# Kernel tuning notes

Hardware: AMD Instinct MI355X
Metric: run time of the kernel (lower is better)

## Reference

```python
import jax, jax.numpy as jnp
import numpy as np

N, E, B = 20000, 320000, 64
IN_DIM, HID, HEADS, NGF = 128, 64, 4, 9
NEG_SLOPE = 0.2
SET2SET_STEPS = 3


def _gat_conv(x, src, dst, W, a_src, a_dst, b, n):
    # PyG GATConv (eval mode): h = xW split into heads, edge score =
    # LeakyReLU(a_src.h[src] + a_dst.h[dst]), softmax over edges per dst node,
    # weighted scatter-sum of h[src], heads concatenated, + bias.
    H, C = a_src.shape
    h = (x @ W).reshape(n, H, C)                       # [N,H,C]
    s = jnp.sum(h * a_src, axis=-1)                    # [N,H]
    d = jnp.sum(h * a_dst, axis=-1)                    # [N,H]
    e = jax.nn.leaky_relu(s[src] + d[dst], NEG_SLOPE)  # [E,H]
    emax = jax.ops.segment_max(e, dst, num_segments=n)
    ex = jnp.exp(e - emax[dst])
    denom = jax.ops.segment_sum(ex, dst, num_segments=n)
    alpha = ex / (denom[dst] + 1e-16)                  # [E,H]
    out = jax.ops.segment_sum(h[src] * alpha[..., None], dst, num_segments=n)
    return out.reshape(n, H * C) + b


def _set2set(x, batch, Wih, Whh, bih, bhh, n_graphs):
    # Set2Set pooling: LSTM(q_star) -> attention over nodes per graph -> readout.
    d = x.shape[1]
    h = jnp.zeros((n_graphs, d), x.dtype)
    c = jnp.zeros((n_graphs, d), x.dtype)
    q_star = jnp.zeros((n_graphs, 2 * d), x.dtype)
    for _ in range(SET2SET_STEPS):
        gates = q_star @ Wih.T + bih + h @ Whh.T + bhh   # [B,4d], torch gate order i,f,g,o
        i, f, g, o = jnp.split(gates, 4, axis=1)
        c = jax.nn.sigmoid(f) * c + jax.nn.sigmoid(i) * jnp.tanh(g)
        h = jax.nn.sigmoid(o) * jnp.tanh(c)
        q = h                                            # [B,d]
        e = jnp.sum(x * q[batch], axis=-1)               # [N]
        emax = jax.ops.segment_max(e, batch, num_segments=n_graphs)
        a = jnp.exp(e - emax[batch])
        a = a / (jax.ops.segment_sum(a, batch, num_segments=n_graphs)[batch] + 1e-16)
        r = jax.ops.segment_sum(a[:, None] * x, batch, num_segments=n_graphs)  # [B,d]
        q_star = jnp.concatenate([q, r], axis=1)
    return q_star


def setup_inputs() -> dict:
    key = jax.random.key(0)
    ks = jax.random.split(key, 20)
    sc = 0.1
    inp = {
        "x": jax.random.normal(ks[0], (N, IN_DIM), jnp.float32),
        "edge_index": jax.random.randint(ks[1], (2, E), 0, N, dtype=jnp.int32),
        "batch": jnp.sort(jax.random.randint(ks[2], (N,), 0, B, dtype=jnp.int32)),
        "graph_features": jax.random.normal(ks[3], (B, NGF), jnp.float32),
        "W1": sc * jax.random.normal(ks[4], (IN_DIM, HEADS * HID), jnp.float32),
        "a_src1": sc * jax.random.normal(ks[5], (HEADS, HID), jnp.float32),
        "a_dst1": sc * jax.random.normal(ks[6], (HEADS, HID), jnp.float32),
        "b1": jnp.zeros((HEADS * HID,), jnp.float32),
        "W2": sc * jax.random.normal(ks[7], (HEADS * HID, HEADS * HID), jnp.float32),
        "a_src2": sc * jax.random.normal(ks[8], (HEADS, HID), jnp.float32),
        "a_dst2": sc * jax.random.normal(ks[9], (HEADS, HID), jnp.float32),
        "b2": jnp.zeros((HEADS * HID,), jnp.float32),
        "W3": sc * jax.random.normal(ks[10], (HEADS * HID, 2 * HID), jnp.float32),
        "a_src3": sc * jax.random.normal(ks[11], (1, 2 * HID), jnp.float32),
        "a_dst3": sc * jax.random.normal(ks[12], (1, 2 * HID), jnp.float32),
        "b3": jnp.zeros((2 * HID,), jnp.float32),
        "Wih": sc * jax.random.normal(ks[13], (4 * 2 * HID, 4 * HID), jnp.float32),
        "Whh": sc * jax.random.normal(ks[14], (4 * 2 * HID, 2 * HID), jnp.float32),
        "bih": jnp.zeros((4 * 2 * HID,), jnp.float32),
        "bhh": jnp.zeros((4 * 2 * HID,), jnp.float32),
        "gW1": sc * jax.random.normal(ks[15], (NGF, HID), jnp.float32),
        "gb1": jnp.zeros((HID,), jnp.float32),
        "gW2": sc * jax.random.normal(ks[16], (HID, HID // 2), jnp.float32),
        "gb2": jnp.zeros((HID // 2,), jnp.float32),
        "mW1": sc * jax.random.normal(ks[17], (2 * (2 * HID) + HID // 2, 128), jnp.float32),
        "mb1": jnp.zeros((128,), jnp.float32),
        "mW2": sc * jax.random.normal(ks[18], (128, 4), jnp.float32),
        "mb2": jnp.zeros((4,), jnp.float32),
    }
    return inp


def reference(x, edge_index, batch, graph_features,
              W1, a_src1, a_dst1, b1,
              W2, a_src2, a_dst2, b2,
              W3, a_src3, a_dst3, b3,
              Wih, Whh, bih, bhh,
              gW1, gb1, gW2, gb2,
              mW1, mb1, mW2, mb2):
    n = x.shape[0]
    # PyG GATConv default add_self_loops=True
    loops = jnp.arange(n, dtype=edge_index.dtype)
    src = jnp.concatenate([edge_index[0], loops])
    dst = jnp.concatenate([edge_index[1], loops])
    h = jax.nn.elu(_gat_conv(x, src, dst, W1, a_src1, a_dst1, b1, n))
    h = jax.nn.elu(_gat_conv(h, src, dst, W2, a_src2, a_dst2, b2, n))
    h = jax.nn.elu(_gat_conv(h, src, dst, W3, a_src3, a_dst3, b3, n))
    pooled = _set2set(h, batch, Wih, Whh, bih, bhh, B)              # [B, 256]
    gf = jax.nn.relu(graph_features @ gW1 + gb1) @ gW2 + gb2        # [B, 32]
    z = jnp.concatenate([pooled, gf], axis=1)                       # [B, 288]
    scores = jax.nn.relu(z @ mW1 + mb1) @ mW2 + mb2                 # [B, 4]
    return scores
```

## Files before the change

### kernel.cpp

```cpp
#include <hip/hip_runtime.h>
#include <hip/hip_bf16.h>
#include <math.h>

#define NEG_SLOPE 0.2f

typedef __attribute__((ext_vector_type(8))) short bf16x8;
typedef __attribute__((ext_vector_type(4))) float f32x4;

__device__ __forceinline__ float sigmoidf(float x){ return 1.f/(1.f+expf(-x)); }
__device__ __forceinline__ float bf2f(unsigned us){ return __uint_as_float(us << 16); }

__device__ __forceinline__ unsigned pack_split(float v){
  __hip_bfloat16 hi = __float2bfloat16(v);
  float rem = v - __bfloat162float(hi);
  __hip_bfloat16 lo = __float2bfloat16(rem);
  unsigned short uh = __builtin_bit_cast(unsigned short, hi);
  unsigned short ul = __builtin_bit_cast(unsigned short, lo);
  return (unsigned)uh | ((unsigned)ul << 16);
}
__device__ __forceinline__ unsigned short bf16of(float v){
  __hip_bfloat16 h = __float2bfloat16(v);
  return __builtin_bit_cast(unsigned short, h);
}

__global__ void init_kernel(int* counts, int* gstart, int* gend,
                            float* rsum, float* lsum, float* sdbuf,
                            int* pad1, int* pad2, int npadints,
                            const float* __restrict__ W1, unsigned* __restrict__ WT1,
                            const float* __restrict__ W2, unsigned* __restrict__ WT2,
                            const float* __restrict__ W3, unsigned* __restrict__ WT3,
                            int n, int b){
  int i = blockIdx.x*blockDim.x + threadIdx.x;
  if (i < n) counts[i] = 0;
  if (i < b){ gstart[i] = 0; gend[i] = 0; }
  if (i < 3*b*128) rsum[i] = 0.f;
  if (i < 3*b) lsum[i] = 0.f;
  if (i < 18*n) sdbuf[i] = 0.f;
  if (i < npadints){ pad1[i] = 0; pad2[i] = 0; }
  if (i < 128*256){
    int k = i>>8, c = i&255;
    WT1[(size_t)c*128 + k] = pack_split(W1[i]);
  }
  if (i < 256*256){
    int k = i>>8, c = i&255;
    WT2[(size_t)c*256 + k] = pack_split(W2[i]);
  }
  if (i < 256*128){
    int k = i>>7, c = i&127;
    WT3[(size_t)c*256 + k] = pack_split(W3[i]);
  }
}

__global__ void build_kernel(const int* __restrict__ ei, const int* __restrict__ batch,
                             int* counts, int* gstart, int* gend, int E, int n){
  int i = blockIdx.x*blockDim.x + threadIdx.x;
  if (i < E) atomicAdd(&counts[ei[E+i]], 1);
  if (i < n){
    int b = batch[i];
    if (i == 0 || batch[i-1] != b) gstart[b] = i;
    if (i == n-1 || batch[i+1] != b) gend[b] = i+1;
  }
}

__global__ void scan_kernel(const int* __restrict__ counts, int* offs, int* cursor, int n){
  const int T = 1024;
  int tid = threadIdx.x;
  int chunk = (n + T - 1)/T;
  int base = tid*chunk;
  int local = 0;
  for (int i=0;i<chunk;i++){ int idx=base+i; if (idx<n) local += counts[idx]; }
  __shared__ int ss[T];
  ss[tid]=local; __syncthreads();
  for (int off=1; off<T; off<<=1){
    int v = (tid>=off)? ss[tid-off] : 0;
    __syncthreads();
    ss[tid]+=v;
    __syncthreads();
  }
  int run = ss[tid]-local;
  for (int i=0;i<chunk;i++){
    int idx=base+i;
    if (idx<n){ offs[idx]=run; cursor[idx]=run; run += counts[idx]; }
  }
  if (tid==T-1) offs[n]=run;
}

__global__ void fill_kernel(const int* __restrict__ ei, int* cursor, int* csr, int E){
  int i = blockIdx.x*blockDim.x + threadIdx.x;
  if (i<E){
    int dst = ei[E+i];
    int pos = atomicAdd(&cursor[dst],1);
    csr[pos] = ei[i];
  }
}

template<bool AF32, int H>
__global__ __launch_bounds__(256) void gemm_bf16(
    const void* __restrict__ Aptr, const short* __restrict__ BT,
    unsigned short* __restrict__ Cb16,
    const float* __restrict__ asrc, const float* __restrict__ adst,
    float* __restrict__ sv, float* __restrict__ dv,
    int M, int Ktot, int N){
  __shared__ short As[64][72];
  __shared__ short Bs[128][72];
  int tid = threadIdx.x;
  int wave = tid>>6, lane = tid&63;
  int quad = lane>>4, l16 = lane&15;
  int bm = blockIdx.y*64, bn = blockIdx.x*128;
  f32x4 acc[8];
  #pragma unroll
  for (int i=0;i<8;i++) acc[i] = (f32x4){0.f,0.f,0.f,0.f};
  int rr = tid>>3;
  int seg = (tid&7)*8;
  int4 ra[2], rb[4];
  auto loadAB = [&](int k0){
    if (AF32){
      const float* A = (const float*)Aptr;
      int Kf = Ktot>>1;
      int fo = (k0+seg)>>1;
      #pragma unroll
      for (int p=0;p<2;p++){
        int row = bm + p*32 + rr;
        float4 v = make_float4(0.f,0.f,0.f,0.f);
        if (row < M) v = *(const float4*)(A + (size_t)row*Kf + fo);
        ra[p] = make_int4((int)pack_split(v.x),(int)pack_split(v.y),
                          (int)pack_split(v.z),(int)pack_split(v.w));
      }
    } else {
      const short* A = (const short*)Aptr;
      #pragma unroll
      for (int p=0;p<2;p++)
        ra[p] = *(const int4*)(A + (size_t)(bm + p*32 + rr)*Ktot + k0 + seg);
    }
    #pragma unroll
    for (int p=0;p<4;p++)
      rb[p] = *(const int4*)(BT + (size_t)(bn + p*32 + rr)*Ktot + k0 + seg);
  };
  loadAB(0);
  for (int k0=0; k0<Ktot; k0+=64){
    __syncthreads();
    #pragma unroll
    for (int p=0;p<2;p++) *(int4*)&As[p*32+rr][seg] = ra[p];
    #pragma unroll
    for (int p=0;p<4;p++) *(int4*)&Bs[p*32+rr][seg] = rb[p];
    __syncthreads();
    if (k0+64 < Ktot) loadAB(k0+64);
    #pragma unroll
    for (int kk=0;kk<2;kk++){
      bf16x8 af = *(bf16x8*)&As[wave*16 + l16][kk*32 + quad*8];
      #pragma unroll
      for (int nf=0;nf<8;nf++){
        bf16x8 bfv = *(bf16x8*)&Bs[nf*16 + l16][kk*32 + quad*8];
        acc[nf] = __builtin_amdgcn_mfma_f32_16x16x32_bf16(af, bfv, acc[nf], 0,0,0);
      }
    }
  }
  float av[8], bv[8];
  #pragma unroll
  for (int nf=0;nf<8;nf++){
    int c = bn + nf*16 + l16;
    av[nf] = asrc[c];
    bv[nf] = adst[c];
  }
  #pragma unroll
  for (int r=0;r<4;r++){
    int row = bm + wave*16 + quad*4 + r;
    float psA=0.f, pdA=0.f, psB=0.f, pdB=0.f;
    #pragma unroll
    for (int nf=0;nf<4;nf++){ psA += acc[nf][r]*av[nf]; pdA += acc[nf][r]*bv[nf]; }
    #pragma unroll
    for (int nf=4;nf<8;nf++){ psB += acc[nf][r]*av[nf]; pdB += acc[nf][r]*bv[nf]; }
    #pragma unroll
    for (int off=1; off<16; off<<=1){
      psA += __shfl_xor(psA,off); pdA += __shfl_xor(pdA,off);
      psB += __shfl_xor(psB,off); pdB += __shfl_xor(pdB,off);
    }
    if (l16==0 && row < M){
      if (H == 4){
        int h0 = bn>>6;
        atomicAdd(&sv[row*4 + h0],     psA);
        atomicAdd(&dv[row*4 + h0],     pdA);
        atomicAdd(&sv[row*4 + h0 + 1], psB);
        atomicAdd(&dv[row*4 + h0 + 1], pdB);
      } else {
        atomicAdd(&sv[row], psA + psB);
        atomicAdd(&dv[row], pdA + pdB);
      }
    }
  }
  __syncthreads();
  unsigned short* stg = (unsigned short*)(&As[0][0]) + wave*528;
  #pragma unroll
  for (int r=0;r<4;r++){
    #pragma unroll
    for (int nf=0;nf<8;nf++)
      stg[quad*132 + nf*16 + l16] = bf16of(acc[nf][r]);
    #pragma unroll
    for (int p=0;p<4;p++){
      int row = bm + wave*16 + p*4 + r;
      if (row < M){
        unsigned v = (unsigned)stg[p*132 + lane*2] |
                     ((unsigned)stg[p*132 + lane*2 + 1] << 16);
        *(unsigned*)(Cb16 + (size_t)row*N + bn + lane*2) = v;
      }
    }
  }
}

template<int H, int C, bool SPLIT>
__global__ __launch_bounds__(256) void agg_kernel(
    const unsigned short* __restrict__ hb, const float* __restrict__ s,
    const float* __restrict__ d, const int* __restrict__ offs,
    const int* __restrict__ csr, const float* __restrict__ bias,
    float* __restrict__ yf, unsigned* __restrict__ ys, int n_nodes){
  constexpr int HC = H*C;
  constexpr int VEC = HC/64;
  int n = blockIdx.x;
  int tid = threadIdx.x;
  int wave = tid>>6, lane = tid&63;
  __shared__ float sdst[H];
  __shared__ float sl[H];
  __shared__ float sw[64*H];
  __shared__ int ssrc[64];
  __shared__ float facc[4][HC];
  if (tid < H) sdst[tid] = d[n*H+tid];
  int start = offs[n];
  int cnt = offs[n+1]-start;
  int cnt1 = cnt+1;
  __syncthreads();
  float acc[VEC] = {};
  float lp[H];
  #pragma unroll
  for (int h=0;h<H;h++) lp[h]=0.f;
  for (int base=0; base<cnt1; base+=64){
    int nchunk = min(64, cnt1-base);
    if (tid < nchunk){
      int i = base+tid;
      int src = (i==cnt) ? n : csr[start+i];
      ssrc[tid]=src;
      if (H == 4){
        float4 sv = *reinterpret_cast<const float4*>(s + (size_t)src*4);
        float ev[4] = {sv.x, sv.y, sv.z, sv.w};
        #pragma unroll
        for (int h=0;h<4;h++){
          float e = ev[h] + sdst[h];
          e = e>=0.f ? e : NEG_SLOPE*e;
          float w = expf(e);
          sw[tid*4+h]=w;
          lp[h]+=w;
        }
      } else {
        float e = s[src] + sdst[0];
        e = e>=0.f ? e : NEG_SLOPE*e;
        float w = expf(e);
        sw[tid]=w;
        lp[0]+=w;
      }
    }
    __syncthreads();
    for (int j=wave; j<nchunk; j+=4){
      int src = ssrc[j];
      const unsigned short* hp = hb + (size_t)src*HC + lane*VEC;
      if (VEC == 4){
        float wt = sw[j*H + (lane>>4)];
        int2 hv = *reinterpret_cast<const int2*>(hp);
        acc[0] += wt*bf2f((unsigned)hv.x & 0xFFFFu);
        acc[1] += wt*bf2f((unsigned)hv.x >> 16);
        acc[2] += wt*bf2f((unsigned)hv.y & 0xFFFFu);
        acc[3] += wt*bf2f((unsigned)hv.y >> 16);
      } else {
        float wt = sw[j];
        unsigned hv = *reinterpret_cast<const unsigned*>(hp);
        acc[0] += wt*bf2f(hv & 0xFFFFu);
        acc[1] += wt*bf2f(hv >> 16);
      }
    }
    __syncthreads();
  }
  if (wave==0){
    #pragma unroll
    for (int off=32; off; off>>=1)
      #pragma unroll
      for (int h=0;h<H;h++) lp[h] += __shfl_down(lp[h],off);
    if (lane==0)
      #pragma unroll
      for (int h=0;h<H;h++) sl[h]=lp[h];
  }
  #pragma unroll
  for (int v=0;v<VEC;v++) facc[wave][lane*VEC+v] = acc[v];
  __syncthreads();
  if (tid < HC){
    float a = facc[0][tid]+facc[1][tid]+facc[2][tid]+facc[3][tid];
    int head = tid / C;
    float o = a/(sl[head]+1e-16f) + bias[tid];
    o = o>0.f ? o : expm1f(o);
    if (SPLIT){
      ys[(size_t)n*HC + tid] = pack_split(o);
    } else {
      yf[(size_t)n*HC + tid] = o;
    }
  }
}

__global__ __launch_bounds__(256) void read_kernel(
    const float* __restrict__ x, const float* __restrict__ q,
    const int* __restrict__ batch,
    float* __restrict__ rsum, float* __restrict__ lsum, int N){
  int tid = threadIdx.x;
  int wave = tid>>6, lane = tid&63;
  int c0 = blockIdx.x*32;
  if (c0 >= N) return;
  __shared__ float ws[32];
  __shared__ int gb[32];
  if (tid < 32 && c0+tid < N) gb[tid] = batch[c0+tid];
  __syncthreads();
  #pragma unroll
  for (int j=0;j<8;j++){
    int k = wave*8 + j;
    int i = c0 + k;
    if (i < N){
      int g = gb[k];
      float2 xv = *reinterpret_cast<const float2*>(x + (size_t)i*128 + lane*2);
      float2 qv = *reinterpret_cast<const float2*>(q + (size_t)g*128 + lane*2);
      float p = xv.x*qv.x + xv.y*qv.y;
      #pragma unroll
      for (int off=32; off; off>>=1) p += __shfl_down(p, off);
      if (lane==0) ws[k] = expf(p);
    }
  }
  __syncthreads();
  if (tid < 128){
    int col = tid;
    int endi = min(c0+32, N);
    int curg = gb[0];
    float acc = 0.f, lacc = 0.f;
    for (int i=c0; i<endi; ++i){
      int g = gb[i-c0];
      if (g != curg){
        atomicAdd(&rsum[curg*128+col], acc);
        if (col==0) atomicAdd(&lsum[curg], lacc);
        acc = 0.f; lacc = 0.f; curg = g;
      }
      float w = ws[i-c0];
      acc += w * x[(size_t)i*128+col];
      lacc += w;
    }
    atomicAdd(&rsum[curg*128+col], acc);
    if (col==0) atomicAdd(&lsum[curg], lacc);
  }
}

template<int STEP>
__global__ __launch_bounds__(256) void s2s_step_kernel(
    const float* __restrict__ rsum, const float* __restrict__ lsum,
    float* __restrict__ hc, float* __restrict__ qbuf,
    const float* __restrict__ Wih, const float* __restrict__ Whh,
    const float* __restrict__ bih, const float* __restrict__ bhh,
    const float* __restrict__ gfeat,
    const float* __restrict__ gW1, const float* __restrict__ gb1,
    const float* __restrict__ gW2, const float* __restrict__ gb2,
    const float* __restrict__ mW1, const float* __restrict__ mb1,
    const float* __restrict__ mW2, const float* __restrict__ mb2,
    float* __restrict__ out, int B){
  int b = blockIdx.x, tid = threadIdx.x;
  __shared__ float qs[256];

  if (STEP > 0){
    if (tid < 128){
      const float* rs = rsum + (size_t)(STEP-1)*B*128 + (size_t)b*128;
      float ls = lsum[(STEP-1)*B + b];
      qs[tid]     = qbuf[b*128+tid];
      qs[128+tid] = rs[tid] / (ls + 1e-16f);
    }
    __syncthreads();
  }

  if (STEP < 3){
    __shared__ float hs[128], gsh[512];
    if (STEP > 0){ if (tid<128) hs[tid] = hc[(size_t)b*128+tid]; }
    __syncthreads();
    #pragma unroll
    for (int p=0;p<2;p++){
      int j = tid + p*256;
      float a = bih[j] + bhh[j];
      if (STEP > 0){
        const float* wi = Wih + (size_t)j*256;
        for (int k=0;k<256;k+=4)
          a += qs[k]*wi[k] + qs[k+1]*wi[k+1] + qs[k+2]*wi[k+2] + qs[k+3]*wi[k+3];
        const float* wh = Whh + (size_t)j*128;
        for (int k=0;k<128;k+=4)
          a += hs[k]*wh[k] + hs[k+1]*wh[k+1] + hs[k+2]*wh[k+2] + hs[k+3]*wh[k+3];
      }
      gsh[j] = a;
    }
    __syncthreads();
    if (tid < 128){
      float cprev = (STEP==0) ? 0.f : hc[(size_t)(B+b)*128+tid];
      float ig = sigmoidf(gsh[tid]);
      float fg = sigmoidf(gsh[128+tid]);
      float gg = tanhf(gsh[256+tid]);
      float og = sigmoidf(gsh[384+tid]);
      float c2 = fg*cprev + ig*gg;
      float h2 = og*tanhf(c2);
      hc[(size_t)b*128+tid] = h2;
      hc[(size_t)(B+b)*128+tid] = c2;
      qbuf[b*128+tid] = h2;
    }
  } else {
    __shared__ float z[288], gf1[64], hid[128];
    z[tid] = qs[tid];
    if (tid < 64){
      float a = gb1[tid];
      for (int k=0;k<9;k++) a += gfeat[b*9+k]*gW1[k*64+tid];
      gf1[tid] = a>0.f ? a : 0.f;
    }
    __syncthreads();
    if (tid < 32){
      float a = gb2[tid];
      for (int k=0;k<64;k++) a += gf1[k]*gW2[k*32+tid];
      z[256+tid] = a;
    }
    __syncthreads();
    if (tid < 128){
      float a = mb1[tid];
      for (int k=0;k<288;k++) a += z[k]*mW1[(size_t)k*128+tid];
      hid[tid] = a>0.f ? a : 0.f;
    }
    __syncthreads();
    if (tid < 4){
      float a = mb2[tid];
      for (int k=0;k<128;k++) a += hid[k]*mW2[k*4+tid];
      out[b*4+tid] = a;
    }
  }
}

extern "C" void kernel_launch(void* const* d_in, const int* in_sizes, int n_in,
                              void* d_out, int out_size, void* d_ws, size_t ws_size,
                              hipStream_t stream) {
  const float* x     = (const float*)d_in[0];
  const int*   ei    = (const int*)d_in[1];
  const int*   batch = (const int*)d_in[2];
  const float* gfeat = (const float*)d_in[3];
  const float* W1    = (const float*)d_in[4];
  const float* as1   = (const float*)d_in[5];
  const float* ad1   = (const float*)d_in[6];
  const float* b1    = (const float*)d_in[7];
  const float* W2    = (const float*)d_in[8];
  const float* as2   = (const float*)d_in[9];
  const float* ad2   = (const float*)d_in[10];
  const float* b2    = (const float*)d_in[11];
  const float* W3    = (const float*)d_in[12];
  const float* as3   = (const float*)d_in[13];
  const float* ad3   = (const float*)d_in[14];
  const float* b3    = (const float*)d_in[15];
  const float* Wih   = (const float*)d_in[16];
  const float* Whh   = (const float*)d_in[17];
  const float* bih   = (const float*)d_in[18];
  const float* bhh   = (const float*)d_in[19];
  const float* gW1   = (const float*)d_in[20];
  const float* gb1   = (const float*)d_in[21];
  const float* gW2   = (const float*)d_in[22];
  const float* gb2   = (const float*)d_in[23];
  const float* mW1   = (const float*)d_in[24];
  const float* mb1   = (const float*)d_in[25];
  const float* mW2   = (const float*)d_in[26];
  const float* mb2   = (const float*)d_in[27];

  const int N = in_sizes[0]/128;
  const int E = in_sizes[1]/2;
  const int B = in_sizes[3]/9;
  const int Mpad = ((N + 127)/128)*128;

  char* ws = (char*)d_ws;
  size_t off = 0;
  auto alloc = [&](size_t bytes)->char*{
    char* p = ws + off;
    off += (bytes + 255) & ~(size_t)255;
    return p;
  };
  unsigned short* hb16 = (unsigned short*)alloc((size_t)N*256*2);
  unsigned* ysplit1 = (unsigned*)alloc((size_t)Mpad*256*4);
  unsigned* ysplit2 = (unsigned*)alloc((size_t)Mpad*256*4);
  float*    ybuf    = (float*)alloc((size_t)N*128*4);
  unsigned* WT1     = (unsigned*)alloc((size_t)256*128*4);
  unsigned* WT2     = (unsigned*)alloc((size_t)256*256*4);
  unsigned* WT3     = (unsigned*)alloc((size_t)128*256*4);
  float* sdbuf  = (float*)alloc((size_t)18*N*4);
  int*   counts = (int*)alloc((size_t)N*4);
  int*   offs   = (int*)alloc((size_t)(N+1)*4);
  int*   cursor = (int*)alloc((size_t)N*4);
  int*   csr    = (int*)alloc((size_t)E*4);
  int*   gstart = (int*)alloc((size_t)B*4);
  int*   gend   = (int*)alloc((size_t)B*4);
  float* hcbuf  = (float*)alloc((size_t)2*B*128*4);
  float* qbuf   = (float*)alloc((size_t)B*128*4);
  float* rsum   = (float*)alloc((size_t)3*B*128*4);
  float* lsum   = (float*)alloc((size_t)3*B*4);

  float* s1 = sdbuf;            float* d1 = sdbuf + (size_t)4*N;
  float* s2 = sdbuf + (size_t)8*N;  float* d2 = sdbuf + (size_t)12*N;
  float* s3 = sdbuf + (size_t)16*N; float* d3 = sdbuf + (size_t)17*N;

  int npadints = (Mpad - N)*256;
  int nInit = 18*N;
  if (npadints > nInit) nInit = npadints;
  if (256*256 > nInit) nInit = 256*256;
  init_kernel<<<(nInit+255)/256, 256, 0, stream>>>(counts, gstart, gend,
      rsum, lsum, sdbuf,
      (int*)(ysplit1 + (size_t)N*256), (int*)(ysplit2 + (size_t)N*256),
      npadints, W1, WT1, W2, WT2, W3, WT3, N, B);
  int gridEN = (max(E,N)+255)/256;
  build_kernel<<<gridEN, 256, 0, stream>>>(ei, batch, counts, gstart, gend, E, N);
  scan_kernel<<<1, 1024, 0, stream>>>(counts, offs, cursor, N);
  fill_kernel<<<(E+255)/256, 256, 0, stream>>>(ei, cursor, csr, E);

  int gm = Mpad/64;
  gemm_bf16<true,4><<<dim3(2,gm), 256, 0, stream>>>((const void*)x, (const short*)WT1,
      hb16, as1, ad1, s1, d1, N, 256, 256);
  agg_kernel<4,64,true><<<N, 256, 0, stream>>>(hb16, s1, d1, offs, csr, b1, nullptr, ysplit1, N);
  gemm_bf16<false,4><<<dim3(2,gm), 256, 0, stream>>>((const void*)ysplit1, (const short*)WT2,
      hb16, as2, ad2, s2, d2, N, 512, 256);
  agg_kernel<4,64,true><<<N, 256, 0, stream>>>(hb16, s2, d2, offs, csr, b2, nullptr, ysplit2, N);
  gemm_bf16<false,1><<<dim3(1,gm), 256, 0, stream>>>((const void*)ysplit2, (const short*)WT3,
      hb16, as3, ad3, s3, d3, N, 512, 128);
  agg_kernel<1,128,false><<<N, 256, 0, stream>>>(hb16, s3, d3, offs, csr, b3, ybuf, nullptr, N);

  int gr = (N+31)/32;
  s2s_step_kernel<0><<<B, 256, 0, stream>>>(rsum, lsum, hcbuf, qbuf,
      Wih, Whh, bih, bhh, gfeat, gW1, gb1, gW2, gb2, mW1, mb1, mW2, mb2, (float*)d_out, B);
  read_kernel<<<gr, 256, 0, stream>>>(ybuf, qbuf, batch, rsum + 0*(size_t)B*128, lsum + 0*B, N);
  s2s_step_kernel<1><<<B, 256, 0, stream>>>(rsum, lsum, hcbuf, qbuf,
      Wih, Whh, bih, bhh, gfeat, gW1, gb1, gW2, gb2, mW1, mb1, mW2, mb2, (float*)d_out, B);
  read_kernel<<<gr, 256, 0, stream>>>(ybuf, qbuf, batch, rsum + 1*(size_t)B*128, lsum + 1*B, N);
  s2s_step_kernel<2><<<B, 256, 0, stream>>>(rsum, lsum, hcbuf, qbuf,
      Wih, Whh, bih, bhh, gfeat, gW1, gb1, gW2, gb2, mW1, mb1, mW2, mb2, (float*)d_out, B);
  read_kernel<<<gr, 256, 0, stream>>>(ybuf, qbuf, batch, rsum + 2*(size_t)B*128, lsum + 2*B, N);
  s2s_step_kernel<3><<<B, 256, 0, stream>>>(rsum, lsum, hcbuf, qbuf,
      Wih, Whh, bih, bhh, gfeat, gW1, gb1, gW2, gb2, mW1, mb1, mW2, mb2, (float*)d_out, B);
}
```

Measured before the change: 524.1 us.

## Restructure GAT aggregation to 32-lane groups per node slice and widen GEMM stores

The aggregation kernel changes from one 256-thread block per node, which needed shared-memory staging and block syncs, to 32-lane groups. Each group handles one node and one 32-channel slice, with edge weights broadcast through warp shuffles and no __syncthreads. This is meant to raise occupancy and cut the sync and reduction overhead for low-degree nodes. In exchange, each slice recomputes the edge exponentials, and each lane now does scalar 2-byte gathers instead of vector loads. The GEMM epilogue also switches to 16-byte row stores through a larger staging area in place of 4-byte stores.

Measured after the change: 572.3 us. +9.2%, slower.

```diff
diff --git a/kernel.cpp b/kernel.cpp
--- a/kernel.cpp
+++ b/kernel.cpp
@@ -189,20 +189,16 @@
     }
   }
   __syncthreads();
-  unsigned short* stg = (unsigned short*)(&As[0][0]) + wave*528;
+  unsigned short* stgS = (unsigned short*)(&As[0][0]) + wave*1056;
   #pragma unroll
   for (int r=0;r<4;r++){
     #pragma unroll
     for (int nf=0;nf<8;nf++)
-      stg[quad*132 + nf*16 + l16] = bf16of(acc[nf][r]);
-    #pragma unroll
-    for (int p=0;p<4;p++){
-      int row = bm + wave*16 + p*4 + r;
-      if (row < M){
-        unsigned v = (unsigned)stg[p*132 + lane*2] |
-                     ((unsigned)stg[p*132 + lane*2 + 1] << 16);
-        *(unsigned*)(Cb16 + (size_t)row*N + bn + lane*2) = v;
-      }
+      stgS[quad*264 + nf*16 + l16] = bf16of(acc[nf][r]);
+    int row = bm + wave*16 + quad*4 + r;
+    if (row < M){
+      int4 v = *(int4*)(stgS + quad*264 + l16*8);
+      *(int4*)(Cb16 + (size_t)row*N + bn + l16*8) = v;
     }
   }
 }
@@ -214,92 +210,45 @@
     const int* __restrict__ csr, const float* __restrict__ bias,
     float* __restrict__ yf, unsigned* __restrict__ ys, int n_nodes){
   constexpr int HC = H*C;
-  constexpr int VEC = HC/64;
-  int n = blockIdx.x;
+  constexpr int SLICES = HC/32;
+  int bx = blockIdx.x;
+  int sl = bx % SLICES;
+  int ng = bx / SLICES;
   int tid = threadIdx.x;
-  int wave = tid>>6, lane = tid&63;
-  __shared__ float sdst[H];
-  __shared__ float sl[H];
-  __shared__ float sw[64*H];
-  __shared__ int ssrc[64];
-  __shared__ float facc[4][HC];
-  if (tid < H) sdst[tid] = d[n*H+tid];
+  int grp = tid >> 5;
+  int l5  = tid & 31;
+  int n = ng*8 + grp;
+  if (n >= n_nodes) return;
+  int c = sl*32 + l5;
+  int head = c / C;
+  float ddst = d[n*H + head];
   int start = offs[n];
-  int cnt = offs[n+1]-start;
-  int cnt1 = cnt+1;
-  __syncthreads();
-  float acc[VEC] = {};
-  float lp[H];
-  #pragma unroll
-  for (int h=0;h<H;h++) lp[h]=0.f;
-  for (int base=0; base<cnt1; base+=64){
-    int nchunk = min(64, cnt1-base);
-    if (tid < nchunk){
-      int i = base+tid;
-      int src = (i==cnt) ? n : csr[start+i];
-      ssrc[tid]=src;
-      if (H == 4){
-        float4 sv = *reinterpret_cast<const float4*>(s + (size_t)src*4);
-        float ev[4] = {sv.x, sv.y, sv.z, sv.w};
-        #pragma unroll
-        for (int h=0;h<4;h++){
-          float e = ev[h] + sdst[h];
-          e = e>=0.f ? e : NEG_SLOPE*e;
-          float w = expf(e);
-          sw[tid*4+h]=w;
-          lp[h]+=w;
-        }
-      } else {
-        float e = s[src] + sdst[0];
-        e = e>=0.f ? e : NEG_SLOPE*e;
-        float w = expf(e);
-        sw[tid]=w;
-        lp[0]+=w;
-      }
-    }
-    __syncthreads();
-    for (int j=wave; j<nchunk; j+=4){
-      int src = ssrc[j];
-      const unsigned short* hp = hb + (size_t)src*HC + lane*VEC;
-      if (VEC == 4){
-        float wt = sw[j*H + (lane>>4)];
-        int2 hv = *reinterpret_cast<const int2*>(hp);
-        acc[0] += wt*bf2f((unsigned)hv.x & 0xFFFFu);
-        acc[1] += wt*bf2f((unsigned)hv.x >> 16);
-        acc[2] += wt*bf2f((unsigned)hv.y & 0xFFFFu);
-        acc[3] += wt*bf2f((unsigned)hv.y >> 16);
-      } else {
-        float wt = sw[j];
-        unsigned hv = *reinterpret_cast<const unsigned*>(hp);
-        acc[0] += wt*bf2f(hv & 0xFFFFu);
-        acc[1] += wt*bf2f(hv >> 16);
-      }
-    }
-    __syncthreads();
-  }
-  if (wave==0){
-    #pragma unroll
-    for (int off=32; off; off>>=1)
-      #pragma unroll
-      for (int h=0;h<H;h++) lp[h] += __shfl_down(lp[h],off);
-    if (lane==0)
-      #pragma unroll
-      for (int h=0;h<H;h++) sl[h]=lp[h];
-  }
-  #pragma unroll
-  for (int v=0;v<VEC;v++) facc[wave][lane*VEC+v] = acc[v];
-  __syncthreads();
-  if (tid < HC){
-    float a = facc[0][tid]+facc[1][tid]+facc[2][tid]+facc[3][tid];
-    int head = tid / C;
-    float o = a/(sl[head]+1e-16f) + bias[tid];
-    o = o>0.f ? o : expm1f(o);
-    if (SPLIT){
-      ys[(size_t)n*HC + tid] = pack_split(o);
-    } else {
-      yf[(size_t)n*HC + tid] = o;
-    }
-  }
+  int cnt = offs[n+1] - start;
+  int cnt1 = cnt + 1;
+  float acc = 0.f, lp = 0.f;
+  for (int base=0; base<cnt1; base+=32){
+    int nchunk = min(32, cnt1-base);
+    int srcv = 0; float wv = 0.f;
+    if (l5 < nchunk){
+      int i = base + l5;
+      srcv = (i==cnt) ? n : csr[start+i];
+      float e = s[srcv*H + head] + ddst;
+      e = e>=0.f ? e : NEG_SLOPE*e;
+      wv = expf(e);
+      lp += wv;
+    }
+    for (int j=0;j<nchunk;j++){
+      int sj = __shfl(srcv, j, 32);
+      float wj = __shfl(wv, j, 32);
+      acc += wj * bf2f((unsigned)hb[(size_t)sj*HC + c]);
+    }
+  }
+  #pragma unroll
+  for (int off=1; off<32; off<<=1) lp += __shfl_xor(lp, off);
+  float o = acc/(lp + 1e-16f) + bias[c];
+  o = o>0.f ? o : expm1f(o);
+  if (SPLIT) ys[(size_t)n*HC + c] = pack_split(o);
+  else       yf[(size_t)n*HC + c] = o;
 }
 
 __global__ __launch_bounds__(256) void read_kernel(
@@ -516,15 +465,16 @@
   fill_kernel<<<(E+255)/256, 256, 0, stream>>>(ei, cursor, csr, E);
 
   int gm = Mpad/64;
+  int ngrp = (N+7)/8;
   gemm_bf16<true,4><<<dim3(2,gm), 256, 0, stream>>>((const void*)x, (const short*)WT1,
       hb16, as1, ad1, s1, d1, N, 256, 256);
-  agg_kernel<4,64,true><<<N, 256, 0, stream>>>(hb16, s1, d1, offs, csr, b1, nullptr, ysplit1, N);
+  agg_kernel<4,64,true><<<ngrp*8, 256, 0, stream>>>(hb16, s1, d1, offs, csr, b1, nullptr, ysplit1, N);
   gemm_bf16<false,4><<<dim3(2,gm), 256, 0, stream>>>((const void*)ysplit1, (const short*)WT2,
       hb16, as2, ad2, s2, d2, N, 512, 256);
-  agg_kernel<4,64,true><<<N, 256, 0, stream>>>(hb16, s2, d2, offs, csr, b2, nullptr, ysplit2, N);
+  agg_kernel<4,64,true><<<ngrp*8, 256, 0, stream>>>(hb16, s2, d2, offs, csr, b2, nullptr, ysplit2, N);
   gemm_bf16<false,1><<<dim3(1,gm), 256, 0, stream>>>((const void*)ysplit2, (const short*)WT3,
       hb16, as3, ad3, s3, d3, N, 512, 128);
-  agg_kernel<1,128,false><<<N, 256, 0, stream>>>(hb16, s3, d3, offs, csr, b3, ybuf, nullptr, N);
+  agg_kernel<1,128,false><<<ngrp*4, 256, 0, stream>>>(hb16, s3, d3, offs, csr, b3, ybuf, nullptr, N);
 
   int gr = (N+31)/32;
   s2s_step_kernel<0><<<B, 256, 0, stream>>>(rsum, lsum, hcbuf, qbuf,
```
